# Performance work log

Hardware: AMD Instinct MI355X
Metric: run time of the kernel (lower is better)

The kernel has to match this reference:

```python
import jax, jax.numpy as jnp
import numpy as np

DIM = 768
NUM_HEADS = 12
HEAD_DIM = DIM // NUM_HEADS
SCALE = HEAD_DIM ** -0.5
B, N = 8, 1024


def setup_inputs() -> dict:
    key = jax.random.key(0)
    k1, k2, k3, k4 = jax.random.split(key, 4)
    s = 1.0 / np.sqrt(DIM)
    return {
        "x": jax.random.normal(k1, (B, N, DIM), dtype=jnp.float32),
        "w_qkv": jax.random.normal(k2, (DIM, 3 * DIM), dtype=jnp.float32) * s,  # qkv_bias=False
        "w_proj": jax.random.normal(k3, (DIM, DIM), dtype=jnp.float32) * s,
        "b_proj": jax.random.normal(k4, (DIM,), dtype=jnp.float32) * 0.01,
    }


def reference(x, w_qkv, w_proj, b_proj):
    Bb, Nn, C = x.shape
    qkv = x @ w_qkv  # [B, N, 3C]
    qkv = qkv.reshape(Bb, Nn, 3, NUM_HEADS, HEAD_DIM)
    q = qkv[:, :, 0].transpose(0, 2, 1, 3)  # [B, H, N, d]
    k = qkv[:, :, 1].transpose(0, 2, 1, 3)
    v = qkv[:, :, 2].transpose(0, 2, 1, 3)
    attn = jnp.einsum("bhqd,bhkd->bhqk", q, k) * SCALE
    attn = jax.nn.softmax(attn, axis=-1)  # dropout p=0 -> identity
    out = jnp.einsum("bhqk,bhkd->bhqd", attn, v)
    out = out.transpose(0, 2, 1, 3).reshape(Bb, Nn, C)
    return out @ w_proj + b_proj
```

## Files before the change

### kernel.cpp

```cpp
#include <hip/hip_runtime.h>
#include <stdint.h>

typedef __attribute__((ext_vector_type(8))) __bf16 bf16x8;
typedef __attribute__((ext_vector_type(8))) unsigned short u16x8;
typedef __attribute__((ext_vector_type(4))) unsigned short u16x4;
typedef __attribute__((ext_vector_type(4))) short s16x4;
typedef __attribute__((ext_vector_type(4))) float f32x4;

typedef unsigned int u32_as1 __attribute__((address_space(1)));
typedef unsigned int u32_as3 __attribute__((address_space(3)));

__device__ __forceinline__ unsigned short f2bf(float f) {
  unsigned int u = __float_as_uint(f);
  u += 0x7fffu + ((u >> 16) & 1u);
  return (unsigned short)(u >> 16);
}

__device__ __forceinline__ bf16x8 ld_frag(const unsigned short* p) {
  return __builtin_bit_cast(bf16x8, *(const u16x8*)p);
}

__device__ __forceinline__ f32x4 mfma16(s16x4 a, s16x4 b, f32x4 c) {
#if __has_builtin(__builtin_amdgcn_mfma_f32_16x16x16bf16_1k)
  return __builtin_amdgcn_mfma_f32_16x16x16bf16_1k(a, b, c, 0, 0, 0);
#elif __has_builtin(__builtin_amdgcn_mfma_f32_16x16x16_bf16_1k)
  return __builtin_amdgcn_mfma_f32_16x16x16_bf16_1k(a, b, c, 0, 0, 0);
#else
  asm volatile("v_mfma_f32_16x16x16_bf16 %0, %1, %2, %0"
               : "+v"(c) : "v"(a), "v"(b));
  return c;
#endif
}

__device__ __forceinline__ float fast_exp2(float x) {
#if __has_builtin(__builtin_amdgcn_exp2f)
  return __builtin_amdgcn_exp2f(x);
#else
  return exp2f(x);
#endif
}

__device__ __forceinline__ void async16(const void* g, void* l) {
  const u32_as1* gp = (const u32_as1*)(uintptr_t)g;
  u32_as3* lp = (u32_as3*)(uintptr_t)l;
  __builtin_amdgcn_global_load_lds(gp, lp, 16, 0, 0);
}

template <int N> __device__ __forceinline__ void wait_vmcnt() {
  if constexpr (N == 0)      asm volatile("s_waitcnt vmcnt(0)" ::: "memory");
  else if constexpr (N == 4) asm volatile("s_waitcnt vmcnt(4)" ::: "memory");
  else if constexpr (N == 5) asm volatile("s_waitcnt vmcnt(5)" ::: "memory");
}

__global__ __launch_bounds__(256) void prep_kernel(
    const float* __restrict__ x, const float* __restrict__ w_qkv,
    const float* __restrict__ w_proj, u16x4* __restrict__ x_bf,
    unsigned short* __restrict__ wqkvT, unsigned short* __restrict__ wprojT) {
  const int bid = blockIdx.x;
  const int t = threadIdx.x;
  if (bid < 6144) {
    const int i = bid * 256 + t;
    float4 v = ((const float4*)x)[i];
    u16x4 o;
    o[0] = f2bf(v.x); o[1] = f2bf(v.y); o[2] = f2bf(v.z); o[3] = f2bf(v.w);
    x_bf[i] = o;
    return;
  }
  __shared__ float tile[32][33];
  const float* w; unsigned short* wt; int N, bx, by;
  if (bid < 6144 + 1728) { const int r = bid - 6144; w = w_qkv; wt = wqkvT; N = 2304; bx = r % 72; by = r / 72; }
  else                   { const int r = bid - 7872; w = w_proj; wt = wprojT; N = 768; bx = r % 24; by = r / 24; }
  const int n0 = bx * 32, k0 = by * 32;
  const int tx = t & 31, ty = t >> 5;
#pragma unroll
  for (int r = 0; r < 4; r++)
    tile[ty + r * 8][tx] = w[(k0 + ty + r * 8) * N + n0 + tx];
  __syncthreads();
#pragma unroll
  for (int r = 0; r < 4; r++)
    wt[(n0 + ty + r * 8) * 768 + k0 + tx] = f2bf(tile[tx][ty + r * 8]);
}

template <int EPI>
__global__ __launch_bounds__(512, 2) void gemm128(
    const unsigned short* __restrict__ A, const unsigned short* __restrict__ Bt,
    unsigned short* __restrict__ qb, unsigned short* __restrict__ kb,
    unsigned short* __restrict__ vtb, float* __restrict__ outp,
    const float* __restrict__ bias) {
  constexpr int NKT = 12;
  constexpr int SSH = 20480;
  __shared__ unsigned short smem[3 * SSH];

  const int t = threadIdx.x;
  const int lane = t & 63, w = t >> 6;
  const int quad = lane >> 4, l15 = lane & 15;
  const int wm = w >> 2, wn = w & 3;

  const int bid = blockIdx.x;
  const int xcd = bid & 7, slot = bid >> 3;
  const int m0 = (xcd * 8 + (slot & 7)) * 128;
  const int n0 = (slot >> 3) * 192;

  const int rs = l15 & 7;
  int arow[4], brow[3], co[2];
#pragma unroll
  for (int i = 0; i < 4; i++) arow[i] = (wm * 64 + i * 16 + l15) * 64;
#pragma unroll
  for (int j = 0; j < 3; j++) brow[j] = 8192 + (wn * 48 + j * 16 + l15) * 64;
#pragma unroll
  for (int kk = 0; kk < 2; kk++) co[kk] = ((kk * 4 + quad) ^ rs) << 3;

  const int srow = t >> 3;
  const int gch = ((t & 7) ^ (srow & 7)) << 3;
  const unsigned short* Ags = A + (m0 + srow) * 768 + gch;
  const unsigned short* Bgs = Bt + (n0 + srow) * 768 + gch;

  f32x4 acc[4][3];
  const f32x4 fzero = {0.f, 0.f, 0.f, 0.f};
#pragma unroll
  for (int i = 0; i < 4; i++)
#pragma unroll
    for (int j = 0; j < 3; j++) acc[i][j] = fzero;

  auto stage = [&](int kt) {
    unsigned short* s = smem + (kt % 3) * SSH + t * 8;
    const int ko = kt * 64;
    async16(Ags + ko, s);
    async16(Ags + 49152 + ko, s + 4096);
    async16(Bgs + ko, s + 8192);
    async16(Bgs + 49152 + ko, s + 12288);
    async16(Bgs + 98304 + ko, s + 16384);
  };

  stage(0);
  stage(1);

#pragma unroll
  for (int kt = 0; kt < NKT; ++kt) {
    if (kt < NKT - 1) wait_vmcnt<5>();
    else              wait_vmcnt<0>();
    __builtin_amdgcn_s_barrier();

    if (kt + 2 < NKT) stage(kt + 2);

    const unsigned short* S = smem + (kt % 3) * SSH;
    bf16x8 af[2][4], bfr[2][3];
#pragma unroll
    for (int kk = 0; kk < 2; kk++) {
#pragma unroll
      for (int i = 0; i < 4; i++) af[kk][i] = ld_frag(S + arow[i] + co[kk]);
#pragma unroll
      for (int j = 0; j < 3; j++) bfr[kk][j] = ld_frag(S + brow[j] + co[kk]);
    }

    __builtin_amdgcn_s_setprio(1);
#pragma unroll
    for (int kk = 0; kk < 2; kk++)
#pragma unroll
      for (int i = 0; i < 4; i++)
#pragma unroll
        for (int j = 0; j < 3; j++)
          acc[i][j] = __builtin_amdgcn_mfma_f32_16x16x32_bf16(af[kk][i], bfr[kk][j], acc[i][j], 0, 0, 0);
    __builtin_amdgcn_s_setprio(0);
  }

  const int which = (n0 >= 1536) ? 2 : (n0 >= 768 ? 1 : 0);
  const int cwb = n0 - which * 768 + wn * 48;
#pragma unroll
  for (int i = 0; i < 4; i++) {
    const int gmb = m0 + wm * 64 + i * 16 + quad * 4;
#pragma unroll
    for (int j = 0; j < 3; j++) {
      const int cw = cwb + j * 16 + l15;
#pragma unroll
      for (int r = 0; r < 4; r++) {
        const int gm = gmb + r;
        float v = acc[i][j][r];
        if (EPI == 0) {
          const int b = gm >> 10, tok = gm & 1023;
          const int h = cw >> 6, d = cw & 63;
          const int bh = b * 12 + h;
          const unsigned short bv = f2bf(v);
          if (which == 0)      qb[(bh << 16) + (tok << 6) + d] = bv;
          else if (which == 1) kb[(bh << 16) + (tok << 6) + d] = bv;
          else                 vtb[(bh << 16) + (d << 10) + tok] = bv;
        } else {
          outp[gm * 768 + n0 + wn * 48 + j * 16 + l15] = v + bias[n0 + wn * 48 + j * 16 + l15];
        }
      }
    }
  }
}

#define SWZC(row, c) (((row) << 6) + ((((c) + (row)) & 7) << 3))
#define C2 0.1803368801111244f

__global__ __launch_bounds__(256, 3) void attn_kernel(
    const unsigned short* __restrict__ qb, const unsigned short* __restrict__ kb,
    const unsigned short* __restrict__ vtb, unsigned short* __restrict__ aout) {
  __shared__ unsigned short smem[3 * 8192];

  const int t = threadIdx.x;
  const int lane = t & 63, w = t >> 6;
  const int quad = lane >> 4, l15 = lane & 15;
  const int bh = blockIdx.x;
  const int b = bh / 12, h = bh - b * 12;
  const int q0 = blockIdx.y * 128;
  const int base = bh << 16;

  bf16x8 qf[2][2];
#pragma unroll
  for (int qt = 0; qt < 2; qt++)
#pragma unroll
    for (int s = 0; s < 2; s++)
      qf[qt][s] = ld_frag(qb + base + ((q0 + w * 32 + qt * 16 + l15) << 6) +
                          s * 32 + quad * 8);

  f32x4 oacc[4][2];
  const f32x4 fzero = {0.f, 0.f, 0.f, 0.f};
#pragma unroll
  for (int dt = 0; dt < 4; dt++) { oacc[dt][0] = fzero; oacc[dt][1] = fzero; }
  float lsum0 = 0.f, lsum1 = 0.f;

  const int srow = t >> 3, schk = t & 7;
  const int c0 = ((schk - srow) & 7) * 8;
  const int c1 = ((schk - (srow + 32)) & 7) * 8;

  auto fillkv = [&](int tile, int buf) {
    const int kv0 = tile * 64;
    unsigned short* Ks = smem + buf * 8192;
    unsigned short* Vts = Ks + 4096;
    async16(kb + base + ((kv0 + srow) << 6) + c0, Ks + t * 8);
    async16(kb + base + ((kv0 + srow + 32) << 6) + c1, Ks + 2048 + t * 8);
    async16(vtb + base + (srow << 10) + kv0 + c0, Vts + t * 8);
    async16(vtb + base + ((srow + 32) << 10) + kv0 + c1, Vts + 2048 + t * 8);
  };

  fillkv(0, 0);
  fillkv(1, 1);
  int cur = 0;
  for (int it = 0; it < 16; ++it) {
    if (it < 15) wait_vmcnt<4>(); else wait_vmcnt<0>();
    asm volatile("s_barrier" ::: "memory");
    if (it + 2 < 16) {
      int tgt = cur + 2; if (tgt >= 3) tgt -= 3;
      fillkv(it + 2, tgt);
    }
    const unsigned short* Ks = smem + cur * 8192;
    const unsigned short* Vts = Ks + 4096;

    f32x4 st[4][2];
#pragma unroll
    for (int tc = 0; tc < 4; tc++) { st[tc][0] = fzero; st[tc][1] = fzero; }
#pragma unroll
    for (int s = 0; s < 2; s++) {
#pragma unroll
      for (int tc = 0; tc < 4; tc++) {
        const bf16x8 kf = ld_frag(Ks + SWZC(tc * 16 + l15, s * 4 + quad));
        st[tc][0] = __builtin_amdgcn_mfma_f32_16x16x32_bf16(kf, qf[0][s], st[tc][0], 0, 0, 0);
        st[tc][1] = __builtin_amdgcn_mfma_f32_16x16x32_bf16(kf, qf[1][s], st[tc][1], 0, 0, 0);
      }
    }

    s16x4 pf[4][2];
#pragma unroll
    for (int tc = 0; tc < 4; tc++) {
#pragma unroll
      for (int qt = 0; qt < 2; qt++) {
        const float p0 = fast_exp2(st[tc][qt][0] * C2);
        const float p1 = fast_exp2(st[tc][qt][1] * C2);
        const float p2 = fast_exp2(st[tc][qt][2] * C2);
        const float p3 = fast_exp2(st[tc][qt][3] * C2);
        const float ps = (p0 + p1) + (p2 + p3);
        if (qt == 0) lsum0 += ps; else lsum1 += ps;
        s16x4 pk;
        pk[0] = (short)f2bf(p0); pk[1] = (short)f2bf(p1);
        pk[2] = (short)f2bf(p2); pk[3] = (short)f2bf(p3);
        pf[tc][qt] = pk;
      }
    }

#pragma unroll
    for (int tc = 0; tc < 4; tc++) {
#pragma unroll
      for (int dt = 0; dt < 4; dt++) {
        const int row = dt * 16 + l15;
        const int addr = (row << 6) + ((((tc * 2 + (quad >> 1)) + row) & 7) << 3) +
                         ((quad & 1) << 2);
        const s16x4 vf = *(const s16x4*)(Vts + addr);
        oacc[dt][0] = mfma16(vf, pf[tc][0], oacc[dt][0]);
        oacc[dt][1] = mfma16(vf, pf[tc][1], oacc[dt][1]);
      }
    }

    cur += 1; if (cur == 3) cur = 0;
  }

  lsum0 += __shfl_xor(lsum0, 16); lsum0 += __shfl_xor(lsum0, 32);
  lsum1 += __shfl_xor(lsum1, 16); lsum1 += __shfl_xor(lsum1, 32);
  const float inv0 = 1.f / lsum0, inv1 = 1.f / lsum1;

  __syncthreads();
  unsigned short* Ot = smem;
#pragma unroll
  for (int dt = 0; dt < 4; dt++) {
#pragma unroll
    for (int qt = 0; qt < 2; qt++) {
      const float inv = qt == 0 ? inv0 : inv1;
      const int qrow = (w * 32 + qt * 16 + l15) * 72 + dt * 16 + quad * 4;
#pragma unroll
      for (int r = 0; r < 4; r++)
        Ot[qrow + r] = f2bf(oacc[dt][qt][r] * inv);
    }
  }
  __syncthreads();
#pragma unroll
  for (int it = 0; it < 4; it++) {
    const int q = it * 32 + (t >> 3);
    const int d0 = (t & 7) * 8;
    const u16x8 v = *(const u16x8*)(Ot + q * 72 + d0);
    *(u16x8*)(aout + (b * 1024 + q0 + q) * 768 + h * 64 + d0) = v;
  }
}

extern "C" void kernel_launch(void* const* d_in, const int* in_sizes, int n_in,
                              void* d_out, int out_size, void* d_ws, size_t ws_size,
                              hipStream_t stream) {
  (void)in_sizes; (void)n_in; (void)out_size; (void)ws_size;
  const float* x = (const float*)d_in[0];
  const float* w_qkv = (const float*)d_in[1];
  const float* w_proj = (const float*)d_in[2];
  const float* b_proj = (const float*)d_in[3];
  float* out = (float*)d_out;

  char* ws = (char*)d_ws;
  unsigned short* x_bf   = (unsigned short*)(ws);
  unsigned short* wqkvT  = (unsigned short*)(ws + 12582912);
  unsigned short* wprojT = (unsigned short*)(ws + 16121856);
  unsigned short* qb     = (unsigned short*)(ws + 17301504);
  unsigned short* kb     = (unsigned short*)(ws + 29884416);
  unsigned short* vtb    = (unsigned short*)(ws + 42467328);
  unsigned short* aout   = x_bf;

  prep_kernel<<<8448, 256, 0, stream>>>(x, w_qkv, w_proj, (u16x4*)x_bf, wqkvT, wprojT);
  gemm128<0><<<768, 512, 0, stream>>>(x_bf, wqkvT, qb, kb, vtb, nullptr, nullptr);
  attn_kernel<<<dim3(96, 8), 256, 0, stream>>>(qb, kb, vtb, aout);
  gemm128<1><<<256, 512, 0, stream>>>(aout, wprojT, nullptr, nullptr, nullptr, out, b_proj);
}
```

Measured before the change: 186.9 us.

## Template GEMM on M-warps, double-buffer LDS, use smaller tiles for projection

```diff
diff --git a/kernel.cpp b/kernel.cpp
--- a/kernel.cpp
+++ b/kernel.cpp
@@ -49,7 +49,6 @@
 template <int N> __device__ __forceinline__ void wait_vmcnt() {
   if constexpr (N == 0)      asm volatile("s_waitcnt vmcnt(0)" ::: "memory");
   else if constexpr (N == 4) asm volatile("s_waitcnt vmcnt(4)" ::: "memory");
-  else if constexpr (N == 5) asm volatile("s_waitcnt vmcnt(5)" ::: "memory");
 }
 
 __global__ __launch_bounds__(256) void prep_kernel(
@@ -81,15 +80,17 @@
     wt[(n0 + ty + r * 8) * 768 + k0 + tx] = f2bf(tile[tx][ty + r * 8]);
 }
 
-template <int EPI>
-__global__ __launch_bounds__(512, 2) void gemm128(
+template <int EPI, int MW>
+__global__ __launch_bounds__(MW * 256, MW * 2) void gemm_bt(
     const unsigned short* __restrict__ A, const unsigned short* __restrict__ Bt,
     unsigned short* __restrict__ qb, unsigned short* __restrict__ kb,
     unsigned short* __restrict__ vtb, float* __restrict__ outp,
     const float* __restrict__ bias) {
   constexpr int NKT = 12;
-  constexpr int SSH = 20480;
-  __shared__ unsigned short smem[3 * SSH];
+  constexpr int BM = MW * 64;
+  constexpr int SSH = (BM + 192) * 64;
+  constexpr int MPX = (MW == 2) ? 8 : 16;
+  __shared__ unsigned short smem[2 * SSH];
 
   const int t = threadIdx.x;
   const int lane = t & 63, w = t >> 6;
@@ -98,15 +99,15 @@
 
   const int bid = blockIdx.x;
   const int xcd = bid & 7, slot = bid >> 3;
-  const int m0 = (xcd * 8 + (slot & 7)) * 128;
-  const int n0 = (slot >> 3) * 192;
+  const int m0 = (xcd * MPX + (slot & (MPX - 1))) * BM;
+  const int n0 = (slot / MPX) * 192;
 
   const int rs = l15 & 7;
   int arow[4], brow[3], co[2];
 #pragma unroll
   for (int i = 0; i < 4; i++) arow[i] = (wm * 64 + i * 16 + l15) * 64;
 #pragma unroll
-  for (int j = 0; j < 3; j++) brow[j] = 8192 + (wn * 48 + j * 16 + l15) * 64;
+  for (int j = 0; j < 3; j++) brow[j] = BM * 64 + (wn * 48 + j * 16 + l15) * 64;
 #pragma unroll
   for (int kk = 0; kk < 2; kk++) co[kk] = ((kk * 4 + quad) ^ rs) << 3;
 
@@ -123,45 +124,50 @@
     for (int j = 0; j < 3; j++) acc[i][j] = fzero;
 
   auto stage = [&](int kt) {
-    unsigned short* s = smem + (kt % 3) * SSH + t * 8;
+    unsigned short* s = smem + (kt & 1) * SSH + t * 8;
     const int ko = kt * 64;
-    async16(Ags + ko, s);
-    async16(Ags + 49152 + ko, s + 4096);
-    async16(Bgs + ko, s + 8192);
-    async16(Bgs + 49152 + ko, s + 12288);
-    async16(Bgs + 98304 + ko, s + 16384);
+    if constexpr (MW == 2) {
+      async16(Ags + ko, s);
+      async16(Ags + 49152 + ko, s + 4096);
+      async16(Bgs + ko, s + 8192);
+      async16(Bgs + 49152 + ko, s + 12288);
+      async16(Bgs + 98304 + ko, s + 16384);
+    } else {
+      async16(Ags + ko, s);
+      async16(Ags + 24576 + ko, s + 2048);
+      async16(Bgs + ko, s + 4096);
+      async16(Bgs + 24576 + ko, s + 6144);
+      async16(Bgs + 49152 + ko, s + 8192);
+      async16(Bgs + 73728 + ko, s + 10240);
+      async16(Bgs + 98304 + ko, s + 12288);
+      async16(Bgs + 122880 + ko, s + 14336);
+    }
   };
 
   stage(0);
-  stage(1);
 
 #pragma unroll
   for (int kt = 0; kt < NKT; ++kt) {
-    if (kt < NKT - 1) wait_vmcnt<5>();
-    else              wait_vmcnt<0>();
+    wait_vmcnt<0>();
     __builtin_amdgcn_s_barrier();
-
-    if (kt + 2 < NKT) stage(kt + 2);
-
-    const unsigned short* S = smem + (kt % 3) * SSH;
-    bf16x8 af[2][4], bfr[2][3];
+    if (kt + 1 < NKT) stage(kt + 1);
+
+    const unsigned short* S = smem + (kt & 1) * SSH;
 #pragma unroll
     for (int kk = 0; kk < 2; kk++) {
-#pragma unroll
-      for (int i = 0; i < 4; i++) af[kk][i] = ld_frag(S + arow[i] + co[kk]);
-#pragma unroll
-      for (int j = 0; j < 3; j++) bfr[kk][j] = ld_frag(S + brow[j] + co[kk]);
-    }
-
-    __builtin_amdgcn_s_setprio(1);
-#pragma unroll
-    for (int kk = 0; kk < 2; kk++)
+      bf16x8 af[4], bfr[3];
+#pragma unroll
+      for (int i = 0; i < 4; i++) af[i] = ld_frag(S + arow[i] + co[kk]);
+#pragma unroll
+      for (int j = 0; j < 3; j++) bfr[j] = ld_frag(S + brow[j] + co[kk]);
+      __builtin_amdgcn_s_setprio(1);
 #pragma unroll
       for (int i = 0; i < 4; i++)
 #pragma unroll
         for (int j = 0; j < 3; j++)
-          acc[i][j] = __builtin_amdgcn_mfma_f32_16x16x32_bf16(af[kk][i], bfr[kk][j], acc[i][j], 0, 0, 0);
-    __builtin_amdgcn_s_setprio(0);
+          acc[i][j] = __builtin_amdgcn_mfma_f32_16x16x32_bf16(af[i], bfr[j], acc[i][j], 0, 0, 0);
+      __builtin_amdgcn_s_setprio(0);
+    }
   }
 
   const int which = (n0 >= 1536) ? 2 : (n0 >= 768 ? 1 : 0);
@@ -343,7 +349,7 @@
   unsigned short* aout   = x_bf;
 
   prep_kernel<<<8448, 256, 0, stream>>>(x, w_qkv, w_proj, (u16x4*)x_bf, wqkvT, wprojT);
-  gemm128<0><<<768, 512, 0, stream>>>(x_bf, wqkvT, qb, kb, vtb, nullptr, nullptr);
+  gemm_bt<0, 2><<<768, 512, 0, stream>>>(x_bf, wqkvT, qb, kb, vtb, nullptr, nullptr);
   attn_kernel<<<dim3(96, 8), 256, 0, stream>>>(qb, kb, vtb, aout);
-  gemm128<1><<<256, 512, 0, stream>>>(aout, wprojT, nullptr, nullptr, nullptr, out, b_proj);
-}
+  gemm_bt<1, 1><<<512, 256, 0, stream>>>(aout, wprojT, nullptr, nullptr, nullptr, out, b_proj);
+}
```

Result: faster. 171.5 us (-8.2%).

## Shrink GEMM tile to 64x192 with K-step 32 and 256-thread blocks

Applied to the files above, without the earlier changes.

```diff
diff --git a/kernel.cpp b/kernel.cpp
--- a/kernel.cpp
+++ b/kernel.cpp
@@ -49,7 +49,6 @@
 template <int N> __device__ __forceinline__ void wait_vmcnt() {
   if constexpr (N == 0)      asm volatile("s_waitcnt vmcnt(0)" ::: "memory");
   else if constexpr (N == 4) asm volatile("s_waitcnt vmcnt(4)" ::: "memory");
-  else if constexpr (N == 5) asm volatile("s_waitcnt vmcnt(5)" ::: "memory");
 }
 
 __global__ __launch_bounds__(256) void prep_kernel(
@@ -82,36 +81,34 @@
 }
 
 template <int EPI>
-__global__ __launch_bounds__(512, 2) void gemm128(
+__global__ __launch_bounds__(256, 3) void gemm_bt(
     const unsigned short* __restrict__ A, const unsigned short* __restrict__ Bt,
     unsigned short* __restrict__ qb, unsigned short* __restrict__ kb,
     unsigned short* __restrict__ vtb, float* __restrict__ outp,
     const float* __restrict__ bias) {
-  constexpr int NKT = 12;
-  constexpr int SSH = 20480;
+  constexpr int NKT = 24;
+  constexpr int SSH = 8192;
   __shared__ unsigned short smem[3 * SSH];
 
   const int t = threadIdx.x;
   const int lane = t & 63, w = t >> 6;
   const int quad = lane >> 4, l15 = lane & 15;
-  const int wm = w >> 2, wn = w & 3;
 
   const int bid = blockIdx.x;
   const int xcd = bid & 7, slot = bid >> 3;
-  const int m0 = (xcd * 8 + (slot & 7)) * 128;
-  const int n0 = (slot >> 3) * 192;
-
-  const int rs = l15 & 7;
-  int arow[4], brow[3], co[2];
-#pragma unroll
-  for (int i = 0; i < 4; i++) arow[i] = (wm * 64 + i * 16 + l15) * 64;
-#pragma unroll
-  for (int j = 0; j < 3; j++) brow[j] = 8192 + (wn * 48 + j * 16 + l15) * 64;
-#pragma unroll
-  for (int kk = 0; kk < 2; kk++) co[kk] = ((kk * 4 + quad) ^ rs) << 3;
-
-  const int srow = t >> 3;
-  const int gch = ((t & 7) ^ (srow & 7)) << 3;
+  const int m0 = (xcd * 16 + (slot & 15)) * 64;
+  const int n0 = (slot >> 4) * 192;
+
+  const int rs = l15 & 3;
+  int arow[4], brow[3];
+#pragma unroll
+  for (int i = 0; i < 4; i++) arow[i] = (i * 16 + l15) * 32;
+#pragma unroll
+  for (int j = 0; j < 3; j++) brow[j] = 2048 + (w * 48 + j * 16 + l15) * 32;
+  const int co = (quad ^ rs) << 3;
+
+  const int srow = t >> 2;
+  const int gch = ((t & 3) ^ (srow & 3)) << 3;
   const unsigned short* Ags = A + (m0 + srow) * 768 + gch;
   const unsigned short* Bgs = Bt + (n0 + srow) * 768 + gch;
 
@@ -124,12 +121,11 @@
 
   auto stage = [&](int kt) {
     unsigned short* s = smem + (kt % 3) * SSH + t * 8;
-    const int ko = kt * 64;
+    const int ko = kt * 32;
     async16(Ags + ko, s);
-    async16(Ags + 49152 + ko, s + 4096);
-    async16(Bgs + ko, s + 8192);
-    async16(Bgs + 49152 + ko, s + 12288);
-    async16(Bgs + 98304 + ko, s + 16384);
+    async16(Bgs + ko, s + 2048);
+    async16(Bgs + 49152 + ko, s + 4096);
+    async16(Bgs + 98304 + ko, s + 6144);
   };
 
   stage(0);
@@ -137,38 +133,33 @@
 
 #pragma unroll
   for (int kt = 0; kt < NKT; ++kt) {
-    if (kt < NKT - 1) wait_vmcnt<5>();
+    if (kt < NKT - 1) wait_vmcnt<4>();
     else              wait_vmcnt<0>();
     __builtin_amdgcn_s_barrier();
 
     if (kt + 2 < NKT) stage(kt + 2);
 
     const unsigned short* S = smem + (kt % 3) * SSH;
-    bf16x8 af[2][4], bfr[2][3];
-#pragma unroll
-    for (int kk = 0; kk < 2; kk++) {
-#pragma unroll
-      for (int i = 0; i < 4; i++) af[kk][i] = ld_frag(S + arow[i] + co[kk]);
-#pragma unroll
-      for (int j = 0; j < 3; j++) bfr[kk][j] = ld_frag(S + brow[j] + co[kk]);
-    }
+    bf16x8 af[4], bfr[3];
+#pragma unroll
+    for (int i = 0; i < 4; i++) af[i] = ld_frag(S + arow[i] + co);
+#pragma unroll
+    for (int j = 0; j < 3; j++) bfr[j] = ld_frag(S + brow[j] + co);
 
     __builtin_amdgcn_s_setprio(1);
 #pragma unroll
-    for (int kk = 0; kk < 2; kk++)
-#pragma unroll
-      for (int i = 0; i < 4; i++)
-#pragma unroll
-        for (int j = 0; j < 3; j++)
-          acc[i][j] = __builtin_amdgcn_mfma_f32_16x16x32_bf16(af[kk][i], bfr[kk][j], acc[i][j], 0, 0, 0);
+    for (int i = 0; i < 4; i++)
+#pragma unroll
+      for (int j = 0; j < 3; j++)
+        acc[i][j] = __builtin_amdgcn_mfma_f32_16x16x32_bf16(af[i], bfr[j], acc[i][j], 0, 0, 0);
     __builtin_amdgcn_s_setprio(0);
   }
 
   const int which = (n0 >= 1536) ? 2 : (n0 >= 768 ? 1 : 0);
-  const int cwb = n0 - which * 768 + wn * 48;
+  const int cwb = n0 - which * 768 + w * 48;
 #pragma unroll
   for (int i = 0; i < 4; i++) {
-    const int gmb = m0 + wm * 64 + i * 16 + quad * 4;
+    const int gmb = m0 + i * 16 + quad * 4;
 #pragma unroll
     for (int j = 0; j < 3; j++) {
       const int cw = cwb + j * 16 + l15;
@@ -185,7 +176,7 @@
           else if (which == 1) kb[(bh << 16) + (tok << 6) + d] = bv;
           else                 vtb[(bh << 16) + (d << 10) + tok] = bv;
         } else {
-          outp[gm * 768 + n0 + wn * 48 + j * 16 + l15] = v + bias[n0 + wn * 48 + j * 16 + l15];
+          outp[gm * 768 + n0 + w * 48 + j * 16 + l15] = v + bias[n0 + w * 48 + j * 16 + l15];
         }
       }
     }
@@ -240,7 +231,8 @@
   fillkv(1, 1);
   int cur = 0;
   for (int it = 0; it < 16; ++it) {
-    if (it < 15) wait_vmcnt<4>(); else wait_vmcnt<0>();
+    if (it < 15) { asm volatile("s_waitcnt vmcnt(4)" ::: "memory"); }
+    else         { asm volatile("s_waitcnt vmcnt(0)" ::: "memory"); }
     asm volatile("s_barrier" ::: "memory");
     if (it + 2 < 16) {
       int tgt = cur + 2; if (tgt >= 3) tgt -= 3;
@@ -343,7 +335,7 @@
   unsigned short* aout   = x_bf;
 
   prep_kernel<<<8448, 256, 0, stream>>>(x, w_qkv, w_proj, (u16x4*)x_bf, wqkvT, wprojT);
-  gemm128<0><<<768, 512, 0, stream>>>(x_bf, wqkvT, qb, kb, vtb, nullptr, nullptr);
+  gemm_bt<0><<<1536, 256, 0, stream>>>(x_bf, wqkvT, qb, kb, vtb, nullptr, nullptr);
   attn_kernel<<<dim3(96, 8), 256, 0, stream>>>(qb, kb, vtb, aout);
-  gemm128<1><<<256, 512, 0, stream>>>(aout, wprojT, nullptr, nullptr, nullptr, out, b_proj);
-}
+  gemm_bt<1><<<512, 256, 0, stream>>>(aout, wprojT, nullptr, nullptr, nullptr, out, b_proj);
+}
```

Result: slower. 195.2 us (+4.4%).

## Add dedicated 64-row GEMM for output projection and raise MFMA priority in attention

Applied to the files above, without the earlier changes.

```diff
diff --git a/kernel.cpp b/kernel.cpp
--- a/kernel.cpp
+++ b/kernel.cpp
@@ -81,12 +81,10 @@
     wt[(n0 + ty + r * 8) * 768 + k0 + tx] = f2bf(tile[tx][ty + r * 8]);
 }
 
-template <int EPI>
 __global__ __launch_bounds__(512, 2) void gemm128(
     const unsigned short* __restrict__ A, const unsigned short* __restrict__ Bt,
     unsigned short* __restrict__ qb, unsigned short* __restrict__ kb,
-    unsigned short* __restrict__ vtb, float* __restrict__ outp,
-    const float* __restrict__ bias) {
+    unsigned short* __restrict__ vtb) {
   constexpr int NKT = 12;
   constexpr int SSH = 20480;
   __shared__ unsigned short smem[3 * SSH];
@@ -172,22 +170,106 @@
 #pragma unroll
     for (int j = 0; j < 3; j++) {
       const int cw = cwb + j * 16 + l15;
+      const int h = cw >> 6, d = cw & 63;
 #pragma unroll
       for (int r = 0; r < 4; r++) {
         const int gm = gmb + r;
-        float v = acc[i][j][r];
-        if (EPI == 0) {
-          const int b = gm >> 10, tok = gm & 1023;
-          const int h = cw >> 6, d = cw & 63;
-          const int bh = b * 12 + h;
-          const unsigned short bv = f2bf(v);
-          if (which == 0)      qb[(bh << 16) + (tok << 6) + d] = bv;
-          else if (which == 1) kb[(bh << 16) + (tok << 6) + d] = bv;
-          else                 vtb[(bh << 16) + (d << 10) + tok] = bv;
-        } else {
-          outp[gm * 768 + n0 + wn * 48 + j * 16 + l15] = v + bias[n0 + wn * 48 + j * 16 + l15];
-        }
+        const int b = gm >> 10, tok = gm & 1023;
+        const int bh = b * 12 + h;
+        const unsigned short bv = f2bf(acc[i][j][r]);
+        if (which == 0)      qb[(bh << 16) + (tok << 6) + d] = bv;
+        else if (which == 1) kb[(bh << 16) + (tok << 6) + d] = bv;
+        else                 vtb[(bh << 16) + (d << 10) + tok] = bv;
       }
+    }
+  }
+}
+
+__global__ __launch_bounds__(256, 2) void gemm64(
+    const unsigned short* __restrict__ A, const unsigned short* __restrict__ Bt,
+    float* __restrict__ outp, const float* __restrict__ bias) {
+  constexpr int NKT = 12;
+  constexpr int SSH = 16384;
+  __shared__ unsigned short smem[2 * SSH];
+
+  const int t = threadIdx.x;
+  const int lane = t & 63, w = t >> 6;
+  const int quad = lane >> 4, l15 = lane & 15;
+
+  const int bid = blockIdx.x;
+  const int xcd = bid & 7, slot = bid >> 3;
+  const int m0 = (xcd * 16 + (slot & 15)) * 64;
+  const int n0 = (slot >> 4) * 192;
+
+  const int rs = l15 & 7;
+  int arow[4], brow[3], co[2];
+#pragma unroll
+  for (int i = 0; i < 4; i++) arow[i] = (i * 16 + l15) * 64;
+#pragma unroll
+  for (int j = 0; j < 3; j++) brow[j] = 4096 + (w * 48 + j * 16 + l15) * 64;
+#pragma unroll
+  for (int kk = 0; kk < 2; kk++) co[kk] = ((kk * 4 + quad) ^ rs) << 3;
+
+  const int srow = t >> 3;
+  const int gch = ((t & 7) ^ (srow & 7)) << 3;
+  const unsigned short* Ags = A + (m0 + srow) * 768 + gch;
+  const unsigned short* Bgs = Bt + (n0 + srow) * 768 + gch;
+
+  f32x4 acc[4][3];
+  const f32x4 fzero = {0.f, 0.f, 0.f, 0.f};
+#pragma unroll
+  for (int i = 0; i < 4; i++)
+#pragma unroll
+    for (int j = 0; j < 3; j++) acc[i][j] = fzero;
+
+  auto stage = [&](int kt) {
+    unsigned short* s = smem + (kt & 1) * SSH + t * 8;
+    const int ko = kt * 64;
+    async16(Ags + ko, s);
+    async16(Ags + 24576 + ko, s + 2048);
+    async16(Bgs + ko, s + 4096);
+    async16(Bgs + 24576 + ko, s + 6144);
+    async16(Bgs + 49152 + ko, s + 8192);
+    async16(Bgs + 73728 + ko, s + 10240);
+    async16(Bgs + 98304 + ko, s + 12288);
+    async16(Bgs + 122880 + ko, s + 14336);
+  };
+
+  stage(0);
+
+#pragma unroll
+  for (int kt = 0; kt < NKT; ++kt) {
+    wait_vmcnt<0>();
+    __builtin_amdgcn_s_barrier();
+    if (kt + 1 < NKT) stage(kt + 1);
+
+    const unsigned short* S = smem + (kt & 1) * SSH;
+#pragma unroll
+    for (int kk = 0; kk < 2; kk++) {
+      bf16x8 af[4], bfr[3];
+#pragma unroll
+      for (int i = 0; i < 4; i++) af[i] = ld_frag(S + arow[i] + co[kk]);
+#pragma unroll
+      for (int j = 0; j < 3; j++) bfr[j] = ld_frag(S + brow[j] + co[kk]);
+      __builtin_amdgcn_s_setprio(1);
+#pragma unroll
+      for (int i = 0; i < 4; i++)
+#pragma unroll
+        for (int j = 0; j < 3; j++)
+          acc[i][j] = __builtin_amdgcn_mfma_f32_16x16x32_bf16(af[i], bfr[j], acc[i][j], 0, 0, 0);
+      __builtin_amdgcn_s_setprio(0);
+    }
+  }
+
+#pragma unroll
+  for (int i = 0; i < 4; i++) {
+    const int gmb = m0 + i * 16 + quad * 4;
+#pragma unroll
+    for (int j = 0; j < 3; j++) {
+      const int gc = n0 + w * 48 + j * 16 + l15;
+#pragma unroll
+      for (int r = 0; r < 4; r++)
+        outp[(gmb + r) * 768 + gc] = acc[i][j][r] + bias[gc];
     }
   }
 }
@@ -240,7 +322,8 @@
   fillkv(1, 1);
   int cur = 0;
   for (int it = 0; it < 16; ++it) {
-    if (it < 15) wait_vmcnt<4>(); else wait_vmcnt<0>();
+    if (it < 15) { asm volatile("s_waitcnt vmcnt(4)" ::: "memory"); }
+    else         { asm volatile("s_waitcnt vmcnt(0)" ::: "memory"); }
     asm volatile("s_barrier" ::: "memory");
     if (it + 2 < 16) {
       int tgt = cur + 2; if (tgt >= 3) tgt -= 3;
@@ -252,6 +335,7 @@
     f32x4 st[4][2];
 #pragma unroll
     for (int tc = 0; tc < 4; tc++) { st[tc][0] = fzero; st[tc][1] = fzero; }
+    __builtin_amdgcn_s_setprio(1);
 #pragma unroll
     for (int s = 0; s < 2; s++) {
 #pragma unroll
@@ -261,6 +345,7 @@
         st[tc][1] = __builtin_amdgcn_mfma_f32_16x16x32_bf16(kf, qf[1][s], st[tc][1], 0, 0, 0);
       }
     }
+    __builtin_amdgcn_s_setprio(0);
 
     s16x4 pf[4][2];
 #pragma unroll
@@ -280,6 +365,7 @@
       }
     }
 
+    __builtin_amdgcn_s_setprio(1);
 #pragma unroll
     for (int tc = 0; tc < 4; tc++) {
 #pragma unroll
@@ -292,6 +378,7 @@
         oacc[dt][1] = mfma16(vf, pf[tc][1], oacc[dt][1]);
       }
     }
+    __builtin_amdgcn_s_setprio(0);
 
     cur += 1; if (cur == 3) cur = 0;
   }
@@ -343,7 +430,7 @@
   unsigned short* aout   = x_bf;
 
   prep_kernel<<<8448, 256, 0, stream>>>(x, w_qkv, w_proj, (u16x4*)x_bf, wqkvT, wprojT);
-  gemm128<0><<<768, 512, 0, stream>>>(x_bf, wqkvT, qb, kb, vtb, nullptr, nullptr);
+  gemm128<<<768, 512, 0, stream>>>(x_bf, wqkvT, qb, kb, vtb);
   attn_kernel<<<dim3(96, 8), 256, 0, stream>>>(qb, kb, vtb, aout);
-  gemm128<1><<<256, 512, 0, stream>>>(aout, wprojT, nullptr, nullptr, nullptr, out, b_proj);
-}
+  gemm64<<<512, 256, 0, stream>>>(aout, wprojT, out, b_proj);
+}
```

New measurement: 179.4 us. 1.04x faster.
